# Optimization experiments

Hardware: AMD Instinct MI355X
Metric: run time of the kernel (lower is better)

The kernel has to match this reference:

```python
import jax, jax.numpy as jnp
import numpy as np

EMBED_DIM = 512
SE_HIDDEN = max(1, int(EMBED_DIM * 0.25))  # 128
LN_EPS = 1e-5


def setup_inputs() -> dict:
    key = jax.random.key(0)
    ks = jax.random.split(key, 16)
    B, H, W, D = 8, 32, 32, EMBED_DIM
    s = 0.02
    return {
        "q": jax.random.normal(ks[0], (B, H, W, D), jnp.float32),
        "k": jax.random.normal(ks[1], (B, H, W, D), jnp.float32),
        "v": jax.random.normal(ks[2], (B, H, W, D), jnp.float32),
        # Linear weights stored as [in, out] (equivalent to torch W.T)
        "Wq": jax.random.normal(ks[3], (D, D), jnp.float32) * s,
        "Wk": jax.random.normal(ks[4], (D, D), jnp.float32) * s,
        "Wv": jax.random.normal(ks[5], (D, D), jnp.float32) * s,
        "Wo": jax.random.normal(ks[6], (D, D), jnp.float32) * s,
        # Conv2d kernel in HWIO layout for NHWC conv
        "conv_w": jax.random.normal(ks[7], (3, 3, D, D), jnp.float32) * s,
        "conv_b": jnp.zeros((D,), jnp.float32),
        "se_w1": jax.random.normal(ks[8], (D, SE_HIDDEN), jnp.float32) * s,
        "se_b1": jnp.zeros((SE_HIDDEN,), jnp.float32),
        "se_w2": jax.random.normal(ks[9], (SE_HIDDEN, D), jnp.float32) * s,
        "se_b2": jnp.zeros((D,), jnp.float32),
        "ln_g": jnp.ones((D,), jnp.float32),
        "ln_b": jnp.zeros((D,), jnp.float32),
    }


def _layernorm(x, g, b):
    mu = jnp.mean(x, axis=-1, keepdims=True)
    var = jnp.mean(jnp.square(x - mu), axis=-1, keepdims=True)
    return (x - mu) * jax.lax.rsqrt(var + LN_EPS) * g + b


def reference(q, k, v, Wq, Wk, Wv, Wo, conv_w, conv_b,
              se_w1, se_b1, se_w2, se_b2, ln_g, ln_b):
    B, H, W, D = q.shape
    scaler = jnp.sqrt(jnp.asarray(D, q.dtype))
    qp = q @ Wq  # [B,H,W,D]
    kp = k @ Wk
    vp = v @ Wv
    N = H * W
    qf = qp.reshape(B, N, D)
    kf = kp.reshape(B, N, D)
    vf = vp.reshape(B, N, D)
    scores = jnp.einsum('bnd,bmd->bnm', qf, kf) / scaler
    probs = jax.nn.softmax(scores, axis=-1)  # dropout p=0 -> identity
    out = jnp.einsum('bnm,bmd->bnd', probs, vf).reshape(B, H, W, D)
    out = out @ Wo
    # 3x3 same conv in NHWC
    out = jax.lax.conv_general_dilated(
        out, conv_w, window_strides=(1, 1), padding='SAME',
        dimension_numbers=('NHWC', 'HWIO', 'NHWC')) + conv_b
    # squeeze-excite: global average pool over spatial dims
    se = jnp.mean(out, axis=(1, 2))  # [B,D]
    se = jax.nn.silu(se @ se_w1 + se_b1)
    se = jax.nn.sigmoid(se @ se_w2 + se_b2)  # [B,D]
    out = out * se[:, None, None, :]
    x = qp + out  # residual uses q AFTER q_proj (q reassigned in torch code)
    return _layernorm(x, ln_g, ln_b)
```

## Files before the change

### kernel.cpp

```cpp
#include <hip/hip_runtime.h>
#include <hip/hip_bf16.h>

using bf16 = __hip_bfloat16;
typedef __attribute__((ext_vector_type(8))) short short8;
typedef __attribute__((ext_vector_type(4))) float f32x4;

static const size_t OFF_QP   = 0;
static const size_t OFF_KP   = (size_t)8  << 20;
static const size_t OFF_VPT  = (size_t)16 << 20;
static const size_t OFF_SC   = (size_t)24 << 20;
static const size_t OFF_PA   = (size_t)40 << 20;
static const size_t OFF_WT   = (size_t)56 << 20;
static const size_t OFF_CWT  = (size_t)58 << 20;
static const size_t OFF_POOL = (size_t)63 << 20;
static const size_t OFF_SE   = ((size_t)63 << 20) + 16384;
static const size_t OFF_RS   = ((size_t)63 << 20) + 32768;

__global__ __launch_bounds__(256) void prep_k(const float* __restrict__ Wq,
                                              const float* __restrict__ Wk,
                                              const float* __restrict__ Wv,
                                              const float* __restrict__ Wo,
                                              const float* __restrict__ convw,
                                              bf16* __restrict__ wT,
                                              bf16* __restrict__ cwT,
                                              float* __restrict__ pooled) {
    long idx = (long)blockIdx.x * 256 + threadIdx.x;
    if (idx < 4l * 262144) {
        int m = (int)(idx >> 18);
        int o = (int)(idx & 262143);
        int n = o >> 9, k = o & 511;
        const float* W = (m == 0) ? Wq : (m == 1) ? Wk : (m == 2) ? Wv : Wo;
        wT[idx] = __float2bfloat16(W[k * 512 + n]);
    } else if (idx < 4l * 262144 + 512l * 4608) {
        long o = idx - 4l * 262144;
        int co = (int)(o / 4608), t = (int)(o % 4608);
        cwT[o] = __float2bfloat16(convw[(long)t * 512 + co]);
    } else if (idx < 4l * 262144 + 512l * 4608 + 4096) {
        pooled[idx - (4l * 262144 + 512l * 4608)] = 0.f;
    }
}

__device__ __forceinline__ float bf2f(unsigned short h) {
    union { unsigned int u; float f; } c;
    c.u = (unsigned int)h << 16;
    return c.f;
}

template <int OP>
__global__ __launch_bounds__(256, 2) void gemm_k(
    const void* __restrict__ Ap0, const void* __restrict__ Ap1, const void* __restrict__ Ap2,
    int lda, long sA,
    const bf16* __restrict__ BT, int ldb, long sB,
    void* __restrict__ Cp, int ldc, long sC,
    int K, float* __restrict__ rs) {
    __shared__ bf16 As[2][128 * 64];
    __shared__ bf16 Bs[2][128 * 64];
    const int tid = threadIdx.x;
    const int l = tid & 63, w = tid >> 6;
    const int wm = w >> 1, wn = w & 1;

    const int gx = gridDim.x, gy = gridDim.y;
    const int nwg = gx * gy * gridDim.z;
    const int bid = blockIdx.x + gx * (blockIdx.y + gy * blockIdx.z);
    const int swz = (bid & 7) * (nwg >> 3) + (bid >> 3);
    const int bx = swz % gx;
    const int rem = swz / gx;
    const int by = rem % gy;
    const int zb = rem / gy;

    const int m0 = by * 128, n0 = bx * 128;
    const float isc = 0.04419417382415922f;

    int kbase = 0;
    const bf16* Ab = nullptr;
    const float* Af = nullptr;
    const bf16* Bb = BT;
    if (OP == 1) {
        Af = (const float*)(zb == 0 ? Ap0 : zb == 1 ? Ap1 : Ap2);
        Bb = BT + (long)zb * 262144;
    } else if (OP == 2) {
        Ab = (const bf16*)Ap0 + (long)zb * sA;
        Bb = BT + (long)zb * sB;
    } else if (OP == 4) {
        Ab = (const bf16*)Ap0 + (long)(zb & 7) * sA;
        Bb = BT + (long)(zb & 7) * sB;
        kbase = (zb >> 3) * 512;
    } else {
        Ab = (const bf16*)Ap0;
    }

    const int fr = l & 15;
    f32x4 acc[4][4] = {};
    float esum[4] = {0.f, 0.f, 0.f, 0.f};

    float rinv_[4];
    if (OP == 5) {
#pragma unroll
        for (int i = 0; i < 4; ++i) {
            int row = m0 + ((tid + i * 256) >> 3);
            rinv_[i] = 1.0f / (rs[row] + rs[8192 + row]);
        }
    }

    short8 ar[4];
    float4 af0[4], af1[4];
    short8 br[4];

    auto stage_load = [&](int t) {
        int k0 = kbase + t * 64;
#pragma unroll
        for (int i = 0; i < 4; ++i) {
            int s = tid + i * 256;
            int row = s >> 3, c = s & 7;
            if (OP == 1) {
                const float* src = Af + (long)(m0 + row) * lda + k0 + c * 8;
                af0[i] = *(const float4*)src;
                af1[i] = *(const float4*)(src + 4);
            } else if (OP == 4) {
                union { short8 s8; unsigned short h[8]; } u, o;
                u.s8 = *(const short8*)(Ab + (long)(m0 + row) * lda + k0 + c * 8);
                float es = 0.f;
#pragma unroll
                for (int j = 0; j < 8; ++j) {
                    float e = __expf(bf2f(u.h[j]));
                    es += e;
                    union { float f; unsigned int ui; } cf;
                    cf.f = e;
                    o.h[j] = (unsigned short)(cf.ui >> 16);
                }
                esum[i] += es;
                ar[i] = o.s8;
            } else if (OP == 5) {
                union { short8 s8; unsigned short h[8]; } u0, u1, o;
                long off = (long)(m0 + row) * lda + k0 + c * 8;
                u0.s8 = *(const short8*)(Ab + off);
                u1.s8 = *(const short8*)(Ab + 4194304 + off);
#pragma unroll
                for (int j = 0; j < 8; ++j) {
                    bf16 b = __float2bfloat16((bf2f(u0.h[j]) + bf2f(u1.h[j])) * rinv_[i]);
                    o.h[j] = *(unsigned short*)&b;
                }
                ar[i] = o.s8;
            } else {
                ar[i] = *(const short8*)(Ab + (long)(m0 + row) * lda + k0 + c * 8);
            }
        }
#pragma unroll
        for (int i = 0; i < 4; ++i) {
            int s = tid + i * 256;
            int row = s >> 3, c = s & 7;
            br[i] = *(const short8*)(Bb + (long)(n0 + row) * ldb + k0 + c * 8);
        }
    };

    auto stage_write = [&](int b) {
#pragma unroll
        for (int i = 0; i < 4; ++i) {
            int s = tid + i * 256;
            int row = s >> 3, c = s & 7;
            int cx = c ^ (row & 7);
            if (OP == 1) {
                union { short8 s8; bf16 h[8]; } u;
                u.h[0] = __float2bfloat16(af0[i].x); u.h[1] = __float2bfloat16(af0[i].y);
                u.h[2] = __float2bfloat16(af0[i].z); u.h[3] = __float2bfloat16(af0[i].w);
                u.h[4] = __float2bfloat16(af1[i].x); u.h[5] = __float2bfloat16(af1[i].y);
                u.h[6] = __float2bfloat16(af1[i].z); u.h[7] = __float2bfloat16(af1[i].w);
                *(short8*)(&As[b][row * 64 + cx * 8]) = u.s8;
            } else {
                *(short8*)(&As[b][row * 64 + cx * 8]) = ar[i];
            }
        }
#pragma unroll
        for (int i = 0; i < 4; ++i) {
            int s = tid + i * 256;
            int row = s >> 3, c = s & 7;
            int cx = c ^ (row & 7);
            *(short8*)(&Bs[b][row * 64 + cx * 8]) = br[i];
        }
    };

    auto compute = [&](int b) {
#pragma unroll
        for (int h = 0; h < 2; ++h) {
            int cx = ((l >> 4) + 4 * h) ^ (fr & 7);
            short8 afr[4], bfv[4];
#pragma unroll
            for (int m = 0; m < 4; ++m) {
                int r = wm * 64 + m * 16 + fr;
                afr[m] = *(const short8*)(&As[b][r * 64 + cx * 8]);
            }
#pragma unroll
            for (int n = 0; n < 4; ++n) {
                int r = wn * 64 + n * 16 + fr;
                bfv[n] = *(const short8*)(&Bs[b][r * 64 + cx * 8]);
            }
#pragma unroll
            for (int m = 0; m < 4; ++m)
#pragma unroll
                for (int n = 0; n < 4; ++n)
                    acc[m][n] = __builtin_amdgcn_mfma_f32_16x16x32_bf16(afr[m], bfv[n], acc[m][n], 0, 0, 0);
        }
    };

    const int nt = K >> 6;
    stage_load(0);
    stage_write(0);
    int cur = 0;
    for (int t = 0; t < nt; ++t) {
        __syncthreads();
        if (t + 1 < nt) stage_load(t + 1);
        compute(cur);
        if (t + 1 < nt) stage_write(cur ^ 1);
        cur ^= 1;
    }

    if (OP == 4) {
        __syncthreads();
        float* fl = (float*)&As[0][0];
#pragma unroll
        for (int i = 0; i < 4; ++i) {
            int s = tid + i * 256;
            fl[(s >> 3) * 8 + (s & 7)] = esum[i];
        }
        __syncthreads();
        if (bx == 0 && tid < 128) {
            float s8 = 0.f;
#pragma unroll
            for (int j = 0; j < 8; ++j) s8 += fl[tid * 8 + j];
            rs[(zb >> 3) * 8192 + (zb & 7) * 1024 + m0 + tid] = s8;
        }
    }

    const int cr = (l >> 4) * 4, cc = l & 15;
#pragma unroll
    for (int m = 0; m < 4; ++m) {
#pragma unroll
        for (int n = 0; n < 4; ++n) {
#pragma unroll
            for (int j = 0; j < 4; ++j) {
                int r = m0 + wm * 64 + m * 16 + cr + j;
                int c = n0 + wn * 64 + n * 16 + cc;
                float vv = acc[m][n][j];
                if (OP == 2) {
                    ((bf16*)Cp)[(long)zb * sC + (long)r * ldc + c] = __float2bfloat16(vv);
                } else if (OP == 4) {
                    ((bf16*)Cp)[(long)(zb >> 3) * 4194304 +
                                ((long)(zb & 7) * 1024 + r) * 512 + c] = __float2bfloat16(vv);
                } else if (OP == 5) {
                    ((bf16*)Cp)[(long)r * ldc + c] = __float2bfloat16(vv);
                } else {
                    if (zb == 2) {
                        ((bf16*)Cp)[(size_t)(OFF_VPT / 2) + ((long)(r >> 10) * 512 + c) * 1024 + (r & 1023)] =
                            __float2bfloat16(vv);
                    } else {
                        float sv = (zb == 1) ? vv * isc : vv;
                        ((bf16*)Cp)[(long)zb * 4194304 + (long)r * 512 + c] = __float2bfloat16(sv);
                    }
                }
            }
        }
    }
}

__global__ __launch_bounds__(256, 4) void conv_k(
    const bf16* __restrict__ A,
    const bf16* __restrict__ BT,
    bf16* __restrict__ P,
    const float* __restrict__ bias,
    float* __restrict__ pooled) {
    __shared__ bf16 As[2][128 * 32];
    __shared__ bf16 Bs[2][128 * 32];
    const int tid = threadIdx.x;
    const int l = tid & 63, w = tid >> 6;
    const int wm = w >> 1, wn = w & 1;

    const int gx = 4, gy = 64, nwg = 1024;
    const int bid = blockIdx.x + gx * (blockIdx.y + gy * blockIdx.z);
    const int swz = (bid & 7) * (nwg >> 3) + (bid >> 3);
    const int bx = swz % gx;
    const int rem = swz / gx;
    const int by = rem % gy;
    const int zb = rem / gy;

    const int m0 = by * 128, n0 = bx * 128;
    const int kbase = zb * 1152;

    const int fr = l & 15;
    const int ck = (l >> 4) ^ ((fr >> 1) & 3);
    f32x4 acc[4][4] = {};

    int pixoff[2], hh_[2], wp_[2];
#pragma unroll
    for (int i = 0; i < 2; ++i) {
        int s = tid + i * 256;
        int row = s >> 2, c = s & 3;
        int p = m0 + row;
        int bb = p >> 10;
        hh_[i] = (p >> 5) & 31;
        wp_[i] = p & 31;
        pixoff[i] = ((bb * 32 + hh_[i]) * 32 + wp_[i]) * 512 + c * 8;
    }

    short8 ar[2], br[2];

    auto stage_load = [&](int t) {
        int k0 = kbase + t * 32;
        int tap = k0 >> 9;
        int dy = tap / 3 - 1, dx = tap % 3 - 1;
        int doff = (dy * 32 + dx) * 512 + (k0 & 511);
#pragma unroll
        for (int i = 0; i < 2; ++i) {
            int h2 = hh_[i] + dy, w2 = wp_[i] + dx;
            if (((unsigned)h2 < 32u) & ((unsigned)w2 < 32u)) {
                ar[i] = *(const short8*)(A + pixoff[i] + doff);
            } else {
                short8 zz = {0, 0, 0, 0, 0, 0, 0, 0};
                ar[i] = zz;
            }
        }
#pragma unroll
        for (int i = 0; i < 2; ++i) {
            int s = tid + i * 256;
            int row = s >> 2, c = s & 3;
            br[i] = *(const short8*)(BT + (long)(n0 + row) * 4608 + k0 + c * 8);
        }
    };

    auto stage_write = [&](int b) {
#pragma unroll
        for (int i = 0; i < 2; ++i) {
            int s = tid + i * 256;
            int row = s >> 2, c = s & 3;
            int c2 = c ^ ((row >> 1) & 3);
            *(short8*)(&As[b][row * 32 + c2 * 8]) = ar[i];
        }
#pragma unroll
        for (int i = 0; i < 2; ++i) {
            int s = tid + i * 256;
            int row = s >> 2, c = s & 3;
            int c2 = c ^ ((row >> 1) & 3);
            *(short8*)(&Bs[b][row * 32 + c2 * 8]) = br[i];
        }
    };

    auto compute = [&](int b) {
        short8 af[4], bf[4];
#pragma unroll
        for (int m = 0; m < 4; ++m) {
            int r = wm * 64 + m * 16 + fr;
            af[m] = *(const short8*)(&As[b][r * 32 + ck * 8]);
        }
#pragma unroll
        for (int n = 0; n < 4; ++n) {
            int r = wn * 64 + n * 16 + fr;
            bf[n] = *(const short8*)(&Bs[b][r * 32 + ck * 8]);
        }
#pragma unroll
        for (int m = 0; m < 4; ++m)
#pragma unroll
            for (int n = 0; n < 4; ++n)
                acc[m][n] = __builtin_amdgcn_mfma_f32_16x16x32_bf16(af[m], bf[n], acc[m][n], 0, 0, 0);
    };

    const int nt = 36;
    stage_load(0);
    stage_write(0);
    int cur = 0;
    for (int t = 0; t < nt; ++t) {
        __syncthreads();
        if (t + 1 < nt) stage_load(t + 1);
        compute(cur);
        if (t + 1 < nt) stage_write(cur ^ 1);
        cur ^= 1;
    }

    const int cr = (l >> 4) * 4, cc = l & 15;
    float csum[4] = {0.f, 0.f, 0.f, 0.f};
#pragma unroll
    for (int m = 0; m < 4; ++m) {
#pragma unroll
        for (int n = 0; n < 4; ++n) {
#pragma unroll
            for (int j = 0; j < 4; ++j) {
                int r = m0 + wm * 64 + m * 16 + cr + j;
                int c = n0 + wn * 64 + n * 16 + cc;
                float vv = acc[m][n][j];
                if (zb == 0) vv += bias[c];
                csum[n] += vv;
                P[(long)zb * 4194304 + (long)r * 512 + c] = __float2bfloat16(vv);
            }
        }
    }
    int bb = m0 >> 10;
#pragma unroll
    for (int n = 0; n < 4; ++n) {
        int c = n0 + wn * 64 + n * 16 + cc;
        atomicAdd(&pooled[bb * 512 + c], csum[n] * (1.0f / 1024.0f));
    }
}

__global__ __launch_bounds__(512) void se_mlp_k(const float* __restrict__ pooled,
                                                const float* __restrict__ w1,
                                                const float* __restrict__ b1,
                                                const float* __restrict__ w2,
                                                const float* __restrict__ b2,
                                                float* __restrict__ se) {
    __shared__ float pl[512];
    __shared__ float part[4][128];
    __shared__ float hid[128];
    const int b = blockIdx.x, t = threadIdx.x;
    pl[t] = pooled[b * 512 + t];
    __syncthreads();
    const int j = t & 127, r = t >> 7;
    float acc = 0.f;
#pragma unroll 8
    for (int s = 0; s < 128; ++s) {
        int i = r * 128 + s;
        acc += pl[i] * w1[i * 128 + j];
    }
    part[r][j] = acc;
    __syncthreads();
    if (t < 128) {
        float a = part[0][t] + part[1][t] + part[2][t] + part[3][t] + b1[t];
        hid[t] = a / (1.f + __expf(-a));
    }
    __syncthreads();
    float acc2 = b2[t];
#pragma unroll 8
    for (int jj = 0; jj < 128; ++jj)
        acc2 += hid[jj] * w2[jj * 512 + t];
    se[b * 512 + t] = 1.f / (1.f + __expf(-acc2));
}

__global__ __launch_bounds__(256) void final_k(const bf16* __restrict__ Pc,
                                               const float* __restrict__ se,
                                               const bf16* __restrict__ qp,
                                               const float* __restrict__ g,
                                               const float* __restrict__ bta,
                                               float* __restrict__ out) {
    __shared__ float red[256];
    long p = blockIdx.x;
    int b = (int)(p >> 10);
    int t = threadIdx.x;
    float x[2];
#pragma unroll
    for (int i = 0; i < 2; ++i) {
        int c = t + i * 256;
        long o = p * 512 + c;
        float cv = __bfloat162float(Pc[o]) + __bfloat162float(Pc[4194304 + o]) +
                   __bfloat162float(Pc[2l * 4194304 + o]) + __bfloat162float(Pc[3l * 4194304 + o]);
        x[i] = __bfloat162float(qp[o]) + cv * se[b * 512 + c];
    }
    red[t] = x[0] + x[1];
    __syncthreads();
    for (int s = 128; s > 0; s >>= 1) {
        if (t < s) red[t] += red[t + s];
        __syncthreads();
    }
    float mu = red[0] * (1.0f / 512.0f);
    __syncthreads();
    float d0 = x[0] - mu, d1 = x[1] - mu;
    red[t] = d0 * d0 + d1 * d1;
    __syncthreads();
    for (int s = 128; s > 0; s >>= 1) {
        if (t < s) red[t] += red[t + s];
        __syncthreads();
    }
    float inv = rsqrtf(red[0] * (1.0f / 512.0f) + 1e-5f);
#pragma unroll
    for (int i = 0; i < 2; ++i) {
        int c = t + i * 256;
        out[p * 512 + c] = (x[i] - mu) * inv * g[c] + bta[c];
    }
}

extern "C" void kernel_launch(void* const* d_in, const int* in_sizes, int n_in,
                              void* d_out, int out_size, void* d_ws, size_t ws_size,
                              hipStream_t stream) {
    const float* q      = (const float*)d_in[0];
    const float* k      = (const float*)d_in[1];
    const float* v      = (const float*)d_in[2];
    const float* Wq     = (const float*)d_in[3];
    const float* Wk     = (const float*)d_in[4];
    const float* Wv     = (const float*)d_in[5];
    const float* Wo     = (const float*)d_in[6];
    const float* convw  = (const float*)d_in[7];
    const float* convb  = (const float*)d_in[8];
    const float* se_w1  = (const float*)d_in[9];
    const float* se_b1  = (const float*)d_in[10];
    const float* se_w2  = (const float*)d_in[11];
    const float* se_b2  = (const float*)d_in[12];
    const float* ln_g   = (const float*)d_in[13];
    const float* ln_b   = (const float*)d_in[14];

    char* ws = (char*)d_ws;
    bf16*  qp     = (bf16*)(ws + OFF_QP);
    bf16*  kp     = (bf16*)(ws + OFF_KP);
    bf16*  vpT    = (bf16*)(ws + OFF_VPT);
    bf16*  out2   = (bf16*)(ws + OFF_VPT);
    bf16*  scores = (bf16*)(ws + OFF_SC);
    bf16*  Pattn  = (bf16*)(ws + OFF_PA);
    bf16*  Pconv  = (bf16*)(ws + OFF_SC);
    bf16*  wT     = (bf16*)(ws + OFF_WT);
    bf16*  cwT    = (bf16*)(ws + OFF_CWT);
    float* pooled = (float*)(ws + OFF_POOL);
    float* se     = (float*)(ws + OFF_SE);
    float* rsums  = (float*)(ws + OFF_RS);

    prep_k<<<13328, 256, 0, stream>>>(Wq, Wk, Wv, Wo, convw, wT, cwT, pooled);

    gemm_k<1><<<dim3(4, 64, 3), 256, 0, stream>>>(q, k, v, 512, 0, wT, 512, 0,
                                                  ws, 512, 0, 512, nullptr);
    gemm_k<2><<<dim3(8, 8, 8), 256, 0, stream>>>(qp, nullptr, nullptr, 512, 1024l * 512,
                                                 kp, 512, 1024l * 512,
                                                 scores, 1024, 1024l * 1024, 512, nullptr);
    gemm_k<4><<<dim3(4, 8, 16), 256, 0, stream>>>(scores, nullptr, nullptr, 1024, 1024l * 1024,
                                                  vpT, 1024, 512l * 1024,
                                                  Pattn, 512, 0, 512, rsums);
    gemm_k<5><<<dim3(4, 64, 1), 256, 0, stream>>>(Pattn, nullptr, nullptr, 512, 0,
                                                  wT + 3 * 262144, 512, 0,
                                                  out2, 512, 0, 512, rsums);
    conv_k<<<dim3(4, 64, 4), 256, 0, stream>>>(out2, cwT, Pconv, convb, pooled);
    se_mlp_k<<<8, 512, 0, stream>>>(pooled, se_w1, se_b1, se_w2, se_b2, se);
    final_k<<<8192, 256, 0, stream>>>(Pconv, se, qp, ln_g, ln_b, (float*)d_out);
}
```

Measured before the change: 221.7 us.

## Drop split-K in conv kernel, use 128x64 tiles with deeper register prefetch

The 3x3 conv implicit GEMM no longer splits K four ways into separate bf16 partial buffers. Each workgroup now computes a 128x64 output tile over the full K=4608 with BK=64, prefetching four stages into registers. The final kernel reads one conv output instead of summing four partials, which removes the partial-buffer write and read traffic. In exchange there are 512 workgroups instead of 1024, so there is less parallelism, plus higher register pressure under launch_bounds(256,2) and a longer serial K loop per block.

```diff
diff --git a/kernel.cpp b/kernel.cpp
--- a/kernel.cpp
+++ b/kernel.cpp
@@ -262,38 +262,33 @@
     }
 }
 
-__global__ __launch_bounds__(256, 4) void conv_k(
+__global__ __launch_bounds__(256, 2) void conv_k(
     const bf16* __restrict__ A,
     const bf16* __restrict__ BT,
-    bf16* __restrict__ P,
+    bf16* __restrict__ C,
     const float* __restrict__ bias,
     float* __restrict__ pooled) {
-    __shared__ bf16 As[2][128 * 32];
-    __shared__ bf16 Bs[2][128 * 32];
+    __shared__ bf16 As[2][128 * 64];
+    __shared__ bf16 Bs[2][64 * 64];
     const int tid = threadIdx.x;
     const int l = tid & 63, w = tid >> 6;
     const int wm = w >> 1, wn = w & 1;
 
-    const int gx = 4, gy = 64, nwg = 1024;
-    const int bid = blockIdx.x + gx * (blockIdx.y + gy * blockIdx.z);
+    const int gx = 8, gy = 64, nwg = 512;
+    const int bid = blockIdx.x + gx * blockIdx.y;
     const int swz = (bid & 7) * (nwg >> 3) + (bid >> 3);
     const int bx = swz % gx;
-    const int rem = swz / gx;
-    const int by = rem % gy;
-    const int zb = rem / gy;
-
-    const int m0 = by * 128, n0 = bx * 128;
-    const int kbase = zb * 1152;
-
+    const int by = swz / gx;
+
+    const int m0 = by * 128, n0 = bx * 64;
     const int fr = l & 15;
-    const int ck = (l >> 4) ^ ((fr >> 1) & 3);
-    f32x4 acc[4][4] = {};
-
-    int pixoff[2], hh_[2], wp_[2];
-#pragma unroll
-    for (int i = 0; i < 2; ++i) {
+    f32x4 acc[4][2] = {};
+
+    int pixoff[4], hh_[4], wp_[4];
+#pragma unroll
+    for (int i = 0; i < 4; ++i) {
         int s = tid + i * 256;
-        int row = s >> 2, c = s & 3;
+        int row = s >> 3, c = s & 7;
         int p = m0 + row;
         int bb = p >> 10;
         hh_[i] = (p >> 5) & 31;
@@ -301,100 +296,117 @@
         pixoff[i] = ((bb * 32 + hh_[i]) * 32 + wp_[i]) * 512 + c * 8;
     }
 
-    short8 ar[2], br[2];
-
-    auto stage_load = [&](int t) {
-        int k0 = kbase + t * 32;
+    struct SR { short8 ar[4]; short8 br[2]; };
+    SR S0, S1, S2, S3;
+
+    auto stage_load = [&](int t, SR& S) {
+        int k0 = t * 64;
         int tap = k0 >> 9;
         int dy = tap / 3 - 1, dx = tap % 3 - 1;
         int doff = (dy * 32 + dx) * 512 + (k0 & 511);
 #pragma unroll
-        for (int i = 0; i < 2; ++i) {
+        for (int i = 0; i < 4; ++i) {
             int h2 = hh_[i] + dy, w2 = wp_[i] + dx;
             if (((unsigned)h2 < 32u) & ((unsigned)w2 < 32u)) {
-                ar[i] = *(const short8*)(A + pixoff[i] + doff);
+                S.ar[i] = *(const short8*)(A + pixoff[i] + doff);
             } else {
                 short8 zz = {0, 0, 0, 0, 0, 0, 0, 0};
-                ar[i] = zz;
+                S.ar[i] = zz;
             }
         }
 #pragma unroll
         for (int i = 0; i < 2; ++i) {
             int s = tid + i * 256;
-            int row = s >> 2, c = s & 3;
-            br[i] = *(const short8*)(BT + (long)(n0 + row) * 4608 + k0 + c * 8);
+            int row = s >> 3, c = s & 7;
+            S.br[i] = *(const short8*)(BT + (long)(n0 + row) * 4608 + k0 + c * 8);
         }
     };
 
-    auto stage_write = [&](int b) {
+    auto stage_write = [&](int b, SR& S) {
+#pragma unroll
+        for (int i = 0; i < 4; ++i) {
+            int s = tid + i * 256;
+            int row = s >> 3, c = s & 7;
+            int cx = c ^ (row & 7);
+            *(short8*)(&As[b][row * 64 + cx * 8]) = S.ar[i];
+        }
 #pragma unroll
         for (int i = 0; i < 2; ++i) {
             int s = tid + i * 256;
-            int row = s >> 2, c = s & 3;
-            int c2 = c ^ ((row >> 1) & 3);
-            *(short8*)(&As[b][row * 32 + c2 * 8]) = ar[i];
-        }
-#pragma unroll
-        for (int i = 0; i < 2; ++i) {
-            int s = tid + i * 256;
-            int row = s >> 2, c = s & 3;
-            int c2 = c ^ ((row >> 1) & 3);
-            *(short8*)(&Bs[b][row * 32 + c2 * 8]) = br[i];
+            int row = s >> 3, c = s & 7;
+            int cx = c ^ (row & 7);
+            *(short8*)(&Bs[b][row * 64 + cx * 8]) = S.br[i];
         }
     };
 
     auto compute = [&](int b) {
-        short8 af[4], bf[4];
-#pragma unroll
-        for (int m = 0; m < 4; ++m) {
-            int r = wm * 64 + m * 16 + fr;
-            af[m] = *(const short8*)(&As[b][r * 32 + ck * 8]);
-        }
-#pragma unroll
-        for (int n = 0; n < 4; ++n) {
-            int r = wn * 64 + n * 16 + fr;
-            bf[n] = *(const short8*)(&Bs[b][r * 32 + ck * 8]);
-        }
-#pragma unroll
-        for (int m = 0; m < 4; ++m)
-#pragma unroll
-            for (int n = 0; n < 4; ++n)
-                acc[m][n] = __builtin_amdgcn_mfma_f32_16x16x32_bf16(af[m], bf[n], acc[m][n], 0, 0, 0);
+#pragma unroll
+        for (int h = 0; h < 2; ++h) {
+            int cx = ((l >> 4) + 4 * h) ^ (fr & 7);
+            short8 afr[4], bfv[2];
+#pragma unroll
+            for (int m = 0; m < 4; ++m) {
+                int r = wm * 64 + m * 16 + fr;
+                afr[m] = *(const short8*)(&As[b][r * 64 + cx * 8]);
+            }
+#pragma unroll
+            for (int n = 0; n < 2; ++n) {
+                int r = wn * 32 + n * 16 + fr;
+                bfv[n] = *(const short8*)(&Bs[b][r * 64 + cx * 8]);
+            }
+#pragma unroll
+            for (int m = 0; m < 4; ++m)
+#pragma unroll
+                for (int n = 0; n < 2; ++n)
+                    acc[m][n] = __builtin_amdgcn_mfma_f32_16x16x32_bf16(afr[m], bfv[n], acc[m][n], 0, 0, 0);
+        }
     };
 
-    const int nt = 36;
-    stage_load(0);
-    stage_write(0);
-    int cur = 0;
-    for (int t = 0; t < nt; ++t) {
-        __syncthreads();
-        if (t + 1 < nt) stage_load(t + 1);
-        compute(cur);
-        if (t + 1 < nt) stage_write(cur ^ 1);
-        cur ^= 1;
+    const int nt = 72;
+    stage_load(0, S0);
+    stage_load(1, S1);
+    stage_load(2, S2);
+    stage_load(3, S3);
+    stage_write(0, S0);
+    for (int t = 0; t < nt; t += 4) {
+        __syncthreads();
+        if (t + 4 < nt) stage_load(t + 4, S0);
+        compute(0);
+        stage_write(1, S1);
+        __syncthreads();
+        if (t + 5 < nt) stage_load(t + 5, S1);
+        compute(1);
+        stage_write(0, S2);
+        __syncthreads();
+        if (t + 6 < nt) stage_load(t + 6, S2);
+        compute(0);
+        stage_write(1, S3);
+        __syncthreads();
+        if (t + 7 < nt) stage_load(t + 7, S3);
+        compute(1);
+        if (t + 4 < nt) stage_write(0, S0);
     }
 
     const int cr = (l >> 4) * 4, cc = l & 15;
-    float csum[4] = {0.f, 0.f, 0.f, 0.f};
+    float csum[2] = {0.f, 0.f};
 #pragma unroll
     for (int m = 0; m < 4; ++m) {
 #pragma unroll
-        for (int n = 0; n < 4; ++n) {
+        for (int n = 0; n < 2; ++n) {
 #pragma unroll
             for (int j = 0; j < 4; ++j) {
                 int r = m0 + wm * 64 + m * 16 + cr + j;
-                int c = n0 + wn * 64 + n * 16 + cc;
-                float vv = acc[m][n][j];
-                if (zb == 0) vv += bias[c];
+                int c = n0 + wn * 32 + n * 16 + cc;
+                float vv = acc[m][n][j] + bias[c];
                 csum[n] += vv;
-                P[(long)zb * 4194304 + (long)r * 512 + c] = __float2bfloat16(vv);
+                C[(long)r * 512 + c] = __float2bfloat16(vv);
             }
         }
     }
     int bb = m0 >> 10;
 #pragma unroll
-    for (int n = 0; n < 4; ++n) {
-        int c = n0 + wn * 64 + n * 16 + cc;
+    for (int n = 0; n < 2; ++n) {
+        int c = n0 + wn * 32 + n * 16 + cc;
         atomicAdd(&pooled[bb * 512 + c], csum[n] * (1.0f / 1024.0f));
     }
 }
@@ -432,7 +444,7 @@
     se[b * 512 + t] = 1.f / (1.f + __expf(-acc2));
 }
 
-__global__ __launch_bounds__(256) void final_k(const bf16* __restrict__ Pc,
+__global__ __launch_bounds__(256) void final_k(const bf16* __restrict__ convo,
                                                const float* __restrict__ se,
                                                const bf16* __restrict__ qp,
                                                const float* __restrict__ g,
@@ -447,9 +459,7 @@
     for (int i = 0; i < 2; ++i) {
         int c = t + i * 256;
         long o = p * 512 + c;
-        float cv = __bfloat162float(Pc[o]) + __bfloat162float(Pc[4194304 + o]) +
-                   __bfloat162float(Pc[2l * 4194304 + o]) + __bfloat162float(Pc[3l * 4194304 + o]);
-        x[i] = __bfloat162float(qp[o]) + cv * se[b * 512 + c];
+        x[i] = __bfloat162float(qp[o]) + __bfloat162float(convo[o]) * se[b * 512 + c];
     }
     red[t] = x[0] + x[1];
     __syncthreads();
@@ -499,8 +509,8 @@
     bf16*  vpT    = (bf16*)(ws + OFF_VPT);
     bf16*  out2   = (bf16*)(ws + OFF_VPT);
     bf16*  scores = (bf16*)(ws + OFF_SC);
+    bf16*  convo  = (bf16*)(ws + OFF_SC);
     bf16*  Pattn  = (bf16*)(ws + OFF_PA);
-    bf16*  Pconv  = (bf16*)(ws + OFF_SC);
     bf16*  wT     = (bf16*)(ws + OFF_WT);
     bf16*  cwT    = (bf16*)(ws + OFF_CWT);
     float* pooled = (float*)(ws + OFF_POOL);
@@ -520,7 +530,7 @@
     gemm_k<5><<<dim3(4, 64, 1), 256, 0, stream>>>(Pattn, nullptr, nullptr, 512, 0,
                                                   wT + 3 * 262144, 512, 0,
                                                   out2, 512, 0, 512, rsums);
-    conv_k<<<dim3(4, 64, 4), 256, 0, stream>>>(out2, cwT, Pconv, convb, pooled);
+    conv_k<<<dim3(8, 64, 1), 256, 0, stream>>>(out2, cwT, convo, convb, pooled);
     se_mlp_k<<<8, 512, 0, stream>>>(pooled, se_w1, se_b1, se_w2, se_b2, se);
-    final_k<<<8192, 256, 0, stream>>>(Pconv, se, qp, ln_g, ln_b, (float*)d_out);
-}
+    final_k<<<8192, 256, 0, stream>>>(convo, se, qp, ln_g, ln_b, (float*)d_out);
+}
```

New measurement: 195.4 us. 11.9% less time.
